# Kernel tuning notes

Hardware: AMD Instinct MI355X
Metric: run time of the kernel (lower is better)

## Reference

```python
import jax, jax.numpy as jnp
import numpy as np

NEG_SLOPE = 0.01  # torch F.leaky_relu default used in the DGL GAT-style layer


def grat_layer(h, src, dst, W, a, n_nodes):
    """One GRAT (GAT-style) layer.
    h: [N, d_in], src/dst: [E] int, W: [d_in, d_out], a: [2*d_out] (attn_fc weight
    on concat [z_src || z_dst]). Returns [N, d_out].
    """
    d_out = W.shape[1]
    z = h @ W                                   # [N, d_out]
    # attention logits per edge: a^T [z_src || z_dst]
    s_src = z @ a[:d_out]                       # [N]
    s_dst = z @ a[d_out:]                       # [N]
    e = jax.nn.leaky_relu(s_src[src] + s_dst[dst], NEG_SLOPE)  # [E]
    # numerically stable softmax over incoming edges of each dst node
    m = jax.ops.segment_max(e, dst, num_segments=n_nodes)      # [N]
    m = jnp.where(jnp.isfinite(m), m, 0.0)      # nodes with no in-edges
    w = jnp.exp(e - m[dst])                     # [E]
    denom = jax.ops.segment_sum(w, dst, num_segments=n_nodes)  # [N]
    alpha = w / jnp.maximum(denom, 1e-9)[dst]   # [E]
    # weighted scatter-aggregate of source features into dst
    out = jax.ops.segment_sum(alpha[:, None] * z[src], dst, num_segments=n_nodes)
    return out                                  # [N, d_out]


def setup_inputs() -> dict:
    key = jax.random.key(0)
    ks = jax.random.split(key, 10)
    N, E = 100000, 1600000
    IN, H1, H2, OUT = 128, 32, 32, 1
    feature = jax.random.normal(ks[0], (N, IN), dtype=jnp.float32)
    src = jax.random.randint(ks[1], (E,), 0, N, dtype=jnp.int32)
    dst = jax.random.randint(ks[2], (E,), 0, N, dtype=jnp.int32)
    s = 0.1
    W1 = jax.random.normal(ks[3], (IN, H1), dtype=jnp.float32) * s
    a1 = jax.random.normal(ks[4], (2 * H1,), dtype=jnp.float32) * s
    W2 = jax.random.normal(ks[5], (H1, H2), dtype=jnp.float32) * s
    a2 = jax.random.normal(ks[6], (2 * H2,), dtype=jnp.float32) * s
    W3 = jax.random.normal(ks[7], (H2, OUT), dtype=jnp.float32) * s
    a3 = jax.random.normal(ks[8], (2 * OUT,), dtype=jnp.float32) * s
    return {"feature": feature, "src": src, "dst": dst,
            "W1": W1, "a1": a1, "W2": W2, "a2": a2, "W3": W3, "a3": a3}


def reference(feature, src, dst, W1, a1, W2, a2, W3, a3):
    n = feature.shape[0]
    h = jax.nn.relu(grat_layer(feature, src, dst, W1, a1, n))
    h = jax.nn.relu(grat_layer(h, src, dst, W2, a2, n))
    h = grat_layer(h, src, dst, W3, a3, n)
    return jax.nn.sigmoid(h)                    # [N, 1]
```

## Files before the change

kernel.cpp:

```cpp
#include <hip/hip_runtime.h>
#include <hip/hip_bf16.h>
#include <cstdint>
#include <cstddef>

#define NEG_SLOPE 0.01f

static __device__ __forceinline__ unsigned short f2bf(float f) {
    __hip_bfloat16 b = __float2bfloat16(f);
    return *(unsigned short*)&b;
}


__global__ __launch_bounds__(128) void gemm1_kernel(
    const float* __restrict__ h, const float* __restrict__ W,
    const float* __restrict__ a, unsigned short* __restrict__ zb,
    float* __restrict__ s_src, float* __restrict__ s_dst, int N)
{
    __shared__ float Wl[128 * 32];
    int tid = threadIdx.x;
    int rowBase = blockIdx.x * 64;

    {
        const float4* W4 = (const float4*)W;
        float4* Wl4 = (float4*)Wl;
        for (int i = tid; i < 1024; i += 128) Wl4[i] = W4[i];
    }
    __syncthreads();

    int wv   = tid >> 6;
    int lane = tid & 63;
    int g    = lane >> 3;
    int l8   = lane & 7;
    int r0   = wv * 32 + g * 4;
    int col4 = l8 * 4;

    float acc[4][4];
#pragma unroll
    for (int i = 0; i < 4; i++)
#pragma unroll
        for (int c = 0; c < 4; c++) acc[i][c] = 0.f;

    const float4* h4  = (const float4*)h;
    const float4* Wl4 = (const float4*)Wl;

    size_t rowOff[4];
#pragma unroll
    for (int i = 0; i < 4; i++) {
        int r = rowBase + r0 + i;
        rowOff[i] = (size_t)((r < N) ? r : (N - 1)) * 32;
    }

#pragma unroll 2
    for (int kq = 0; kq < 32; kq++) {
        float4 w0 = Wl4[(kq * 4 + 0) * 8 + l8];
        float4 w1 = Wl4[(kq * 4 + 1) * 8 + l8];
        float4 w2 = Wl4[(kq * 4 + 2) * 8 + l8];
        float4 w3 = Wl4[(kq * 4 + 3) * 8 + l8];
#pragma unroll
        for (int i = 0; i < 4; i++) {
            float4 hv = h4[rowOff[i] + kq];
            acc[i][0] += hv.x * w0.x; acc[i][1] += hv.x * w0.y;
            acc[i][2] += hv.x * w0.z; acc[i][3] += hv.x * w0.w;
            acc[i][0] += hv.y * w1.x; acc[i][1] += hv.y * w1.y;
            acc[i][2] += hv.y * w1.z; acc[i][3] += hv.y * w1.w;
            acc[i][0] += hv.z * w2.x; acc[i][1] += hv.z * w2.y;
            acc[i][2] += hv.z * w2.z; acc[i][3] += hv.z * w2.w;
            acc[i][0] += hv.w * w3.x; acc[i][1] += hv.w * w3.y;
            acc[i][2] += hv.w * w3.z; acc[i][3] += hv.w * w3.w;
        }
    }

    float4 alo = ((const float4*)a)[l8];
    float4 ahi = ((const float4*)a)[8 + l8];
#pragma unroll
    for (int i = 0; i < 4; i++) {
        int row = rowBase + r0 + i;
        if (row < N) {
            ushort4 zv4 = make_ushort4(f2bf(acc[i][0]), f2bf(acc[i][1]),
                                       f2bf(acc[i][2]), f2bf(acc[i][3]));
            *(ushort4*)&zb[(size_t)row * 32 + col4] = zv4;
            float ps = acc[i][0] * alo.x + acc[i][1] * alo.y + acc[i][2] * alo.z + acc[i][3] * alo.w;
            float pd = acc[i][0] * ahi.x + acc[i][1] * ahi.y + acc[i][2] * ahi.z + acc[i][3] * ahi.w;
            ps += __shfl_xor(ps, 1, 64); ps += __shfl_xor(ps, 2, 64); ps += __shfl_xor(ps, 4, 64);
            pd += __shfl_xor(pd, 1, 64); pd += __shfl_xor(pd, 2, 64); pd += __shfl_xor(pd, 4, 64);
            if (l8 == 0) { s_src[row] = ps; s_dst[row] = pd; }
        }
    }
}


#define TILE_E 4096
#define NB_MAX 512

__global__ __launch_bounds__(256) void csr_hist_kernel(
    const int* __restrict__ dst, int* __restrict__ counts,
    int E, int TB, int NB)
{
    __shared__ int hist[NB_MAX];
    int tid = threadIdx.x;
    int t = blockIdx.x;
    for (int b = tid; b < NB; b += 256) hist[b] = 0;
    __syncthreads();
    int base = t * TILE_E;
    for (int i = tid; i < TILE_E; i += 256) {
        int k = base + i;
        if (k < E) atomicAdd(&hist[dst[k] >> 8], 1);
    }
    __syncthreads();
    for (int b = tid; b < NB; b += 256) counts[b * TB + t] = hist[b];
}

__global__ __launch_bounds__(256) void scan1_kernel(
    const int* __restrict__ vals, int* __restrict__ incl,
    int* __restrict__ blockSums, int M)
{
    __shared__ int tmp[256];
    int tid = threadIdx.x;
    int i = blockIdx.x * 256 + tid;
    int v = (i < M) ? vals[i] : 0;
    tmp[tid] = v;
    __syncthreads();
#pragma unroll
    for (int off = 1; off < 256; off <<= 1) {
        int t = (tid >= off) ? tmp[tid - off] : 0;
        __syncthreads();
        tmp[tid] += t;
        __syncthreads();
    }
    if (i < M) incl[i] = tmp[tid];
    if (tid == 255) blockSums[blockIdx.x] = tmp[255];
}

__global__ __launch_bounds__(256) void scan3_kernel(
    const int* __restrict__ vals, const int* __restrict__ blockSums,
    int* __restrict__ cscan, int M, int E)
{
    __shared__ int red[256];
    int tid = threadIdx.x;
    int bid = blockIdx.x;
    int partial = 0;
    for (int j = tid; j < bid; j += 256) partial += blockSums[j];
    red[tid] = partial;
    __syncthreads();
#pragma unroll
    for (int off = 128; off > 0; off >>= 1) {
        if (tid < off) red[tid] += red[tid + off];
        __syncthreads();
    }
    int prefix = red[0];
    int i = bid * 256 + tid;
    if (i < M) cscan[i] = cscan[i] - vals[i] + prefix;
    if (i == 0) cscan[M] = E;
}

__global__ __launch_bounds__(256) void csr_scatter_kernel(
    const int* __restrict__ src, const int* __restrict__ dst,
    const int* __restrict__ cscan, int* __restrict__ ebuf,
    int E, int TB, int NB)
{
    __shared__ int baseB[NB_MAX];
    __shared__ int cur[NB_MAX];
    int tid = threadIdx.x;
    int t = blockIdx.x;
    for (int b = tid; b < NB; b += 256) {
        baseB[b] = cscan[b * TB + t];
        cur[b] = 0;
    }
    __syncthreads();
    int base = t * TILE_E;
    for (int i = tid; i < TILE_E; i += 256) {
        int k = base + i;
        if (k < E) {
            int d = dst[k], s = src[k];
            int b = d >> 8;
            int r = atomicAdd(&cur[b], 1);
            ebuf[baseB[b] + r] = (s << 8) | (d & 255);
        }
    }
}

__global__ __launch_bounds__(256) void csr_bucket_kernel(
    const int* __restrict__ ebuf, const int* __restrict__ cscan,
    int* __restrict__ csr_src, int* __restrict__ offsets,
    int N, int E, int TB)
{
    __shared__ int eb[8192];
    __shared__ int hist[256];
    __shared__ int loff[256];
    __shared__ int tmp[256];
    int tid = threadIdx.x;
    int b = blockIdx.x;

    int beg = cscan[b * TB];
    int endv = cscan[(b + 1) * TB];
    int cnt = endv - beg;
    int first = b << 8;

    hist[tid] = 0;
    __syncthreads();

    bool inLds = (cnt <= 8192);
    for (int i = tid; i < cnt; i += 256) {
        int v = ebuf[beg + i];
        if (inLds) eb[i] = v;
        atomicAdd(&hist[v & 255], 1);
    }
    __syncthreads();

    int hv = hist[tid];
    tmp[tid] = hv;
    __syncthreads();
#pragma unroll
    for (int off = 1; off < 256; off <<= 1) {
        int t = (tid >= off) ? tmp[tid - off] : 0;
        __syncthreads();
        tmp[tid] += t;
        __syncthreads();
    }
    loff[tid] = tmp[tid] - hv;
    __syncthreads();

    if (first + tid < N) offsets[first + tid] = beg + loff[tid];
    if (b == 0 && tid == 0) offsets[N] = E;

    hist[tid] = 0;
    __syncthreads();

    for (int i = tid; i < cnt; i += 256) {
        int v = inLds ? eb[i] : ebuf[beg + i];
        int d8 = v & 255;
        int r = atomicAdd(&hist[d8], 1);
        csr_src[beg + loff[d8] + r] = v >> 8;
    }
}


#define AGG32_CORE(S_SRC, S_DST, ZB)                                          \
    int beg = offsets[node], end = offsets[node + 1];                         \
    int deg = end - beg;                                                      \
    float sd = (S_DST)[node];                                                 \
    int q  = lane >> 3;                                                       \
    int c4 = (lane & 7) * 4;                                                  \
    unsigned cb = (unsigned)(lane & 7) * 8u;                                  \
    const char* zbc = (const char*)(ZB);                                      \
    float4 o4 = make_float4(0.f, 0.f, 0.f, 0.f);                              \
    float rden;                                                               \
    if (deg <= 32) {                                                          \
        int p = beg + lane;                                                   \
        int vld = (p < end);                                                  \
        int s = vld ? csr_src[p] : 0;                                         \
        float sval = (S_SRC)[s];            \
        int soff = s << 6;                                                    \
        int e0 = __shfl(soff, q + 0,  32);                                    \
        int e1 = __shfl(soff, q + 4,  32);                                    \
        int e2 = __shfl(soff, q + 8,  32);                                    \
        int e3 = __shfl(soff, q + 12, 32);                                    \
        uint2 g0 = *(const uint2*)(zbc + (cb + (unsigned)e0));                \
        uint2 g1 = *(const uint2*)(zbc + (cb + (unsigned)e1));                \
        uint2 g2 = *(const uint2*)(zbc + (cb + (unsigned)e2));                \
        uint2 g3 = *(const uint2*)(zbc + (cb + (unsigned)e3));                \
        float e = -3.0e38f;                                                   \
        if (vld) {                                                            \
            e = sval + sd;                                                    \
            e = (e > 0.f) ? e : NEG_SLOPE * e;                                \
        }                                                                     \
        float m = e;                                                          \
        _Pragma("unroll")                                                     \
        for (int off = 16; off > 0; off >>= 1)                                \
            m = fmaxf(m, __shfl_xor(m, off, 32));                             \
        float w = vld ? __expf(e - m) : 0.f;                                  \
        float l = w;                                                          \
        _Pragma("unroll")                                                     \
        for (int off = 16; off > 0; off >>= 1) l += __shfl_xor(l, off, 32);   \
        rden = 1.f / fmaxf(l, 1e-9f);                                         \
        uint2 g4, g5, g6, g7;                                                 \
        if (deg > 16) {         \
            int e4 = __shfl(soff, q + 16, 32);                                \
            int e5 = __shfl(soff, q + 20, 32);                                \
            int e6 = __shfl(soff, q + 24, 32);                                \
            int e7 = __shfl(soff, q + 28, 32);                                \
            g4 = *(const uint2*)(zbc + (cb + (unsigned)e4));                  \
            g5 = *(const uint2*)(zbc + (cb + (unsigned)e5));                  \
            g6 = *(const uint2*)(zbc + (cb + (unsigned)e6));                  \
            g7 = *(const uint2*)(zbc + (cb + (unsigned)e7));                  \
        }                                                                     \
        float w0 = __shfl(w, q + 0,  32);                                     \
        float w1 = __shfl(w, q + 4,  32);                                     \
        float w2 = __shfl(w, q + 8,  32);                                     \
        float w3 = __shfl(w, q + 12, 32);                                     \
        o4.x += w0 * __uint_as_float(g0.x << 16);                             \
        o4.y += w0 * __uint_as_float(g0.x & 0xffff0000u);                     \
        o4.z += w0 * __uint_as_float(g0.y << 16);                             \
        o4.w += w0 * __uint_as_float(g0.y & 0xffff0000u);                     \
        o4.x += w1 * __uint_as_float(g1.x << 16);                             \
        o4.y += w1 * __uint_as_float(g1.x & 0xffff0000u);                     \
        o4.z += w1 * __uint_as_float(g1.y << 16);                             \
        o4.w += w1 * __uint_as_float(g1.y & 0xffff0000u);                     \
        o4.x += w2 * __uint_as_float(g2.x << 16);                             \
        o4.y += w2 * __uint_as_float(g2.x & 0xffff0000u);                     \
        o4.z += w2 * __uint_as_float(g2.y << 16);                             \
        o4.w += w2 * __uint_as_float(g2.y & 0xffff0000u);                     \
        o4.x += w3 * __uint_as_float(g3.x << 16);                             \
        o4.y += w3 * __uint_as_float(g3.x & 0xffff0000u);                     \
        o4.z += w3 * __uint_as_float(g3.y << 16);                             \
        o4.w += w3 * __uint_as_float(g3.y & 0xffff0000u);                     \
        if (deg > 16) {                                                       \
            float w4 = __shfl(w, q + 16, 32);                                 \
            float w5 = __shfl(w, q + 20, 32);                                 \
            float w6 = __shfl(w, q + 24, 32);                                 \
            float w7 = __shfl(w, q + 28, 32);                                 \
            o4.x += w4 * __uint_as_float(g4.x << 16);                         \
            o4.y += w4 * __uint_as_float(g4.x & 0xffff0000u);                 \
            o4.z += w4 * __uint_as_float(g4.y << 16);                         \
            o4.w += w4 * __uint_as_float(g4.y & 0xffff0000u);                 \
            o4.x += w5 * __uint_as_float(g5.x << 16);                         \
            o4.y += w5 * __uint_as_float(g5.x & 0xffff0000u);                 \
            o4.z += w5 * __uint_as_float(g5.y << 16);                         \
            o4.w += w5 * __uint_as_float(g5.y & 0xffff0000u);                 \
            o4.x += w6 * __uint_as_float(g6.x << 16);                         \
            o4.y += w6 * __uint_as_float(g6.x & 0xffff0000u);                 \
            o4.z += w6 * __uint_as_float(g6.y << 16);                         \
            o4.w += w6 * __uint_as_float(g6.y & 0xffff0000u);                 \
            o4.x += w7 * __uint_as_float(g7.x << 16);                         \
            o4.y += w7 * __uint_as_float(g7.x & 0xffff0000u);                 \
            o4.z += w7 * __uint_as_float(g7.y << 16);                         \
            o4.w += w7 * __uint_as_float(g7.y & 0xffff0000u);                 \
        }                                                                     \
    } else if (deg <= 128) {                                                  \
        int   sreg[4];                                                        \
        float ev[4];                                                          \
        int nIter = (deg + 31) >> 5;                                          \
        float m = -3.0e38f;                                                   \
        _Pragma("unroll 4")                                                   \
        for (int it = 0; it < nIter; ++it) {                                  \
            int p = beg + it * 32 + lane;                                     \
            float e = -3.0e38f;                                               \
            int s = 0;                                                        \
            if (p < end) {                                                    \
                s = csr_src[p];                                               \
                e = (S_SRC)[s] + sd;                                          \
                e = (e > 0.f) ? e : NEG_SLOPE * e;                            \
            }                                                                 \
            sreg[it] = s << 6;                                                \
            ev[it] = e;                                                       \
            m = fmaxf(m, e);                                                  \
        }                                                                     \
        _Pragma("unroll")                                                     \
        for (int off = 16; off > 0; off >>= 1)                                \
            m = fmaxf(m, __shfl_xor(m, off, 32));                             \
        float l = 0.f;                                                        \
        _Pragma("unroll 4")                                                   \
        for (int it = 0; it < nIter; ++it) {                                  \
            int p = beg + it * 32 + lane;                                     \
            float w = (p < end) ? __expf(ev[it] - m) : 0.f;                   \
            ws[it * 32 + lane] = make_float2(w, __int_as_float(sreg[it]));    \
            l += w;                                                           \
        }                                                                     \
        _Pragma("unroll")                                                     \
        for (int off = 16; off > 0; off >>= 1) l += __shfl_xor(l, off, 32);   \
        rden = 1.f / fmaxf(l, 1e-9f);                                         \
        int degP = (deg + 3) & ~3;                                            \
        int p = 0;                                                            \
        for (; p + 16 <= degP; p += 16) {                                     \
            float2 a0 = ws[p +      q], a1 = ws[p + 4  + q];                  \
            float2 a2 = ws[p + 8  + q], a3 = ws[p + 12 + q];                  \
            uint2 u0 = *(const uint2*)(zbc + (cb + (unsigned)__float_as_int(a0.y))); \
            uint2 u1 = *(const uint2*)(zbc + (cb + (unsigned)__float_as_int(a1.y))); \
            uint2 u2 = *(const uint2*)(zbc + (cb + (unsigned)__float_as_int(a2.y))); \
            uint2 u3 = *(const uint2*)(zbc + (cb + (unsigned)__float_as_int(a3.y))); \
            o4.x += a0.x * __uint_as_float(u0.x << 16);                       \
            o4.y += a0.x * __uint_as_float(u0.x & 0xffff0000u);               \
            o4.z += a0.x * __uint_as_float(u0.y << 16);                       \
            o4.w += a0.x * __uint_as_float(u0.y & 0xffff0000u);               \
            o4.x += a1.x * __uint_as_float(u1.x << 16);                       \
            o4.y += a1.x * __uint_as_float(u1.x & 0xffff0000u);               \
            o4.z += a1.x * __uint_as_float(u1.y << 16);                       \
            o4.w += a1.x * __uint_as_float(u1.y & 0xffff0000u);               \
            o4.x += a2.x * __uint_as_float(u2.x << 16);                       \
            o4.y += a2.x * __uint_as_float(u2.x & 0xffff0000u);               \
            o4.z += a2.x * __uint_as_float(u2.y << 16);                       \
            o4.w += a2.x * __uint_as_float(u2.y & 0xffff0000u);               \
            o4.x += a3.x * __uint_as_float(u3.x << 16);                       \
            o4.y += a3.x * __uint_as_float(u3.x & 0xffff0000u);               \
            o4.z += a3.x * __uint_as_float(u3.y << 16);                       \
            o4.w += a3.x * __uint_as_float(u3.y & 0xffff0000u);               \
        }                                                                     \
        for (; p < degP; p += 4) {                                            \
            float2 aa = ws[p + q];                                            \
            uint2 u = *(const uint2*)(zbc + (cb + (unsigned)__float_as_int(aa.y))); \
            o4.x += aa.x * __uint_as_float(u.x << 16);                        \
            o4.y += aa.x * __uint_as_float(u.x & 0xffff0000u);                \
            o4.z += aa.x * __uint_as_float(u.y << 16);                        \
            o4.w += aa.x * __uint_as_float(u.y & 0xffff0000u);                \
        }                                                                     \
    } else {                                                                  \
        float m = -3.0e38f;                                                   \
        for (int p = beg + lane; p < end; p += 32) {                          \
            float e = (S_SRC)[csr_src[p]] + sd;                               \
            e = (e > 0.f) ? e : NEG_SLOPE * e;                                \
            m = fmaxf(m, e);                                                  \
        }                                                                     \
        _Pragma("unroll")                                                     \
        for (int off = 16; off > 0; off >>= 1)                                \
            m = fmaxf(m, __shfl_xor(m, off, 32));                             \
        float l = 0.f;                                                        \
        for (int p = beg + lane; p < end; p += 32) {                          \
            float e = (S_SRC)[csr_src[p]] + sd;                               \
            e = (e > 0.f) ? e : NEG_SLOPE * e;                                \
            l += __expf(e - m);                                               \
        }                                                                     \
        _Pragma("unroll")                                                     \
        for (int off = 16; off > 0; off >>= 1) l += __shfl_xor(l, off, 32);   \
        rden = 1.f / fmaxf(l, 1e-9f);                                         \
        for (int p = 0; p < deg; p += 4) {                                    \
            int idx = p + q;                                                  \
            int valid = (idx < deg);                                          \
            int s = csr_src[beg + (valid ? idx : deg - 1)];                   \
            float e = (S_SRC)[s] + sd;                                        \
            e = (e > 0.f) ? e : NEG_SLOPE * e;                                \
            float w = valid ? __expf(e - m) : 0.f;                            \
            uint2 u = *(const uint2*)(zbc + (cb + ((unsigned)s << 6)));       \
            o4.x += w * __uint_as_float(u.x << 16);                           \
            o4.y += w * __uint_as_float(u.x & 0xffff0000u);                   \
            o4.z += w * __uint_as_float(u.y << 16);                           \
            o4.w += w * __uint_as_float(u.y & 0xffff0000u);                   \
        }                                                                     \
    }                                                                         \
    o4.x += __shfl_xor(o4.x, 8, 32);                                          \
    o4.y += __shfl_xor(o4.y, 8, 32);                                          \
    o4.z += __shfl_xor(o4.z, 8, 32);                                          \
    o4.w += __shfl_xor(o4.w, 8, 32);                                          \
    o4.x += __shfl_xor(o4.x, 16, 32);                                         \
    o4.y += __shfl_xor(o4.y, 16, 32);                                         \
    o4.z += __shfl_xor(o4.z, 16, 32);                                         \
    o4.w += __shfl_xor(o4.w, 16, 32);                                         \
    float4 vv4;                                                               \
    vv4.x = fmaxf(o4.x * rden, 0.f);                                          \
    vv4.y = fmaxf(o4.y * rden, 0.f);                                          \
    vv4.z = fmaxf(o4.z * rden, 0.f);                                          \
    vv4.w = fmaxf(o4.w * rden, 0.f);

__global__ __launch_bounds__(256) void agg32_l1_kernel(
    const int* __restrict__ offsets, const int* __restrict__ csr_src,
    const float* __restrict__ s_src1, const float* __restrict__ s_dst1,
    const unsigned short* __restrict__ zb1,
    const float* __restrict__ W2, const float* __restrict__ a2,
    unsigned short* __restrict__ zb2,
    float* __restrict__ s_src2, float* __restrict__ s_dst2, int N)
{
    __shared__ float W2l[32 * 32];
    __shared__ float2 wsbuf[8 * 128];
    __shared__ float hl[8 * 32];
    int tid = threadIdx.x;
    for (int i = tid; i < 1024; i += 256) W2l[i] = W2[i];
    __syncthreads();

    int g    = tid >> 5;
    int lane = tid & 31;
    int node = blockIdx.x * 8 + g;
    if (node >= N) return;
    float2* ws = &wsbuf[g * 128];

    AGG32_CORE(s_src1, s_dst1, zb1)

    if (q == 0) *(float4*)&hl[g * 32 + c4] = vv4;
    const float4* hb4 = (const float4*)&hl[g * 32];
    float acc2 = 0.f;
#pragma unroll
    for (int c = 0; c < 8; ++c) {
        float4 hv = hb4[c];
        acc2 += hv.x * W2l[(c * 4 + 0) * 32 + lane];
        acc2 += hv.y * W2l[(c * 4 + 1) * 32 + lane];
        acc2 += hv.z * W2l[(c * 4 + 2) * 32 + lane];
        acc2 += hv.w * W2l[(c * 4 + 3) * 32 + lane];
    }

    zb2[(size_t)node * 32 + lane] = f2bf(acc2);
    float ps = acc2 * a2[lane];
    float pd = acc2 * a2[32 + lane];
#pragma unroll
    for (int off = 16; off > 0; off >>= 1) {
        ps += __shfl_xor(ps, off, 32);
        pd += __shfl_xor(pd, off, 32);
    }
    if (lane == 0) { s_src2[node] = ps; s_dst2[node] = pd; }
}

__global__ __launch_bounds__(256) void agg32_l2_kernel(
    const int* __restrict__ offsets, const int* __restrict__ csr_src,
    const float* __restrict__ s_src2, const float* __restrict__ s_dst2,
    const unsigned short* __restrict__ zb2,
    const float* __restrict__ W3, const float* __restrict__ a3,
    float2* __restrict__ zs, float* __restrict__ s_dst3, int N)
{
    __shared__ float2 wsbuf[8 * 128];
    int tid  = threadIdx.x;
    int g    = tid >> 5;
    int lane = tid & 31;
    int node = blockIdx.x * 8 + g;
    if (node >= N) return;
    float2* ws = &wsbuf[g * 128];

    AGG32_CORE(s_src2, s_dst2, zb2)

    float4 w3q = ((const float4*)W3)[lane & 7];
    float t = vv4.x * w3q.x + vv4.y * w3q.y + vv4.z * w3q.z + vv4.w * w3q.w;
    t += __shfl_xor(t, 1, 32);
    t += __shfl_xor(t, 2, 32);
    t += __shfl_xor(t, 4, 32);
    if (lane == 0) {
        zs[node] = make_float2(t, t * a3[0]);
        s_dst3[node] = t * a3[1];
    }
}

__global__ __launch_bounds__(256) void agg1_fused_kernel(
    const int* __restrict__ offsets, const int* __restrict__ csr_src,
    const float2* __restrict__ zs, const float* __restrict__ s_dst,
    float* __restrict__ out, int N)
{
    int node = blockIdx.x * 8 + (threadIdx.x >> 5);
    int lane = threadIdx.x & 31;
    if (node >= N) return;

    int beg = offsets[node], end = offsets[node + 1];
    int deg = end - beg;
    float sd = s_dst[node];

    if (deg <= 128) {
        float ev[4], zv[4];
        int nIter = (deg + 31) >> 5;
        float m = -3.0e38f;
#pragma unroll 4
        for (int it = 0; it < nIter; ++it) {
            int p = beg + it * 32 + lane;
            float e = -3.0e38f, zz = 0.f;
            if (p < end) {
                float2 v2 = zs[csr_src[p]];
                zz = v2.x;
                e = v2.y + sd;
                e = (e > 0.f) ? e : NEG_SLOPE * e;
            }
            ev[it] = e; zv[it] = zz;
            m = fmaxf(m, e);
        }
#pragma unroll
        for (int off = 16; off > 0; off >>= 1) m = fmaxf(m, __shfl_xor(m, off, 32));
        float l = 0.f, o = 0.f;
#pragma unroll 4
        for (int it = 0; it < nIter; ++it) {
            int p = beg + it * 32 + lane;
            float w = (p < end) ? __expf(ev[it] - m) : 0.f;
            l += w;
            o += w * zv[it];
        }
#pragma unroll
        for (int off = 16; off > 0; off >>= 1) {
            l += __shfl_xor(l, off, 32);
            o += __shfl_xor(o, off, 32);
        }
        if (lane == 0) {
            float v = o / fmaxf(l, 1e-9f);
            out[node] = 1.f / (1.f + __expf(-v));
        }
    } else {
        float m = -3.0e38f;
        for (int p = beg + lane; p < end; p += 32) {
            float e = zs[csr_src[p]].y + sd;
            e = (e > 0.f) ? e : NEG_SLOPE * e;
            m = fmaxf(m, e);
        }
#pragma unroll
        for (int off = 16; off > 0; off >>= 1) m = fmaxf(m, __shfl_xor(m, off, 32));
        float l = 0.f, o = 0.f;
        for (int p = beg + lane; p < end; p += 32) {
            float2 v2 = zs[csr_src[p]];
            float e = v2.y + sd;
            e = (e > 0.f) ? e : NEG_SLOPE * e;
            float w = __expf(e - m);
            l += w; o += w * v2.x;
        }
#pragma unroll
        for (int off = 16; off > 0; off >>= 1) {
            l += __shfl_xor(l, off, 32);
            o += __shfl_xor(o, off, 32);
        }
        if (lane == 0) {
            float v = o / fmaxf(l, 1e-9f);
            out[node] = 1.f / (1.f + __expf(-v));
        }
    }
}


extern "C" void kernel_launch(void* const* d_in, const int* in_sizes, int n_in,
                              void* d_out, int out_size, void* d_ws, size_t ws_size,
                              hipStream_t stream)
{
    const float* feature = (const float*)d_in[0];
    const int*   src     = (const int*)d_in[1];
    const int*   dst     = (const int*)d_in[2];
    const float* W1      = (const float*)d_in[3];
    const float* a1      = (const float*)d_in[4];
    const float* W2      = (const float*)d_in[5];
    const float* a2      = (const float*)d_in[6];
    const float* W3      = (const float*)d_in[7];
    const float* a3      = (const float*)d_in[8];
    float* out = (float*)d_out;

    const int N = in_sizes[0] / 128;
    const int E = in_sizes[1];

    const int TB = (E + TILE_E - 1) / TILE_E;
    const int NB = (N + 255) >> 8;
    const int M  = NB * TB;

    char* p = (char*)d_ws;
    unsigned short* zb1 = (unsigned short*)p;  p += (size_t)N * 32 * sizeof(unsigned short);
    unsigned short* zb2 = (unsigned short*)p;  p += (size_t)N * 32 * sizeof(unsigned short);
    float* zs32    = (float*)p;  p += (size_t)N * 2 * sizeof(float);
    float* s_src1  = (float*)p;  p += (size_t)N * sizeof(float);
    float* s_dst1  = (float*)p;  p += (size_t)N * sizeof(float);
    float* s_src2  = (float*)p;  p += (size_t)N * sizeof(float);
    float* s_dst2  = (float*)p;  p += (size_t)N * sizeof(float);
    float* s_dst3  = (float*)p;  p += (size_t)N * sizeof(float);
    int*   offsets = (int*)p;    p += ((size_t)N + 1) * sizeof(int);
    int*   counts  = (int*)p;    p += ((size_t)M + 1) * sizeof(int);
    int*   cscan   = (int*)p;    p += ((size_t)M + 1) * sizeof(int);
    int*   blockSums = (int*)p;  p += 1024 * sizeof(int);
    int*   ebuf    = (int*)p;    p += (size_t)E * sizeof(int);
    int*   csr_src = (int*)p;    p += (size_t)E * sizeof(int);

    const int nodeBlocks8  = (N + 7) / 8;
    const int gemmBlocks64 = (N + 63) / 64;
    const int scanBlocksM  = (M + 255) / 256;

    hipLaunchKernelGGL(csr_hist_kernel, dim3(TB), dim3(256), 0, stream,
                       dst, counts, E, TB, NB);
    hipLaunchKernelGGL(scan1_kernel, dim3(scanBlocksM), dim3(256), 0, stream,
                       counts, cscan, blockSums, M);
    hipLaunchKernelGGL(scan3_kernel, dim3(scanBlocksM), dim3(256), 0, stream,
                       counts, blockSums, cscan, M, E);
    hipLaunchKernelGGL(csr_scatter_kernel, dim3(TB), dim3(256), 0, stream,
                       src, dst, cscan, ebuf, E, TB, NB);
    hipLaunchKernelGGL(csr_bucket_kernel, dim3(NB), dim3(256), 0, stream,
                       ebuf, cscan, csr_src, offsets, N, E, TB);

    hipLaunchKernelGGL(gemm1_kernel, dim3(gemmBlocks64), dim3(128), 0, stream,
                       feature, W1, a1, zb1, s_src1, s_dst1, N);
    hipLaunchKernelGGL(agg32_l1_kernel, dim3(nodeBlocks8), dim3(256), 0, stream,
                       offsets, csr_src, s_src1, s_dst1, zb1, W2, a2,
                       zb2, s_src2, s_dst2, N);

    float2* zs = (float2*)zs32;
    hipLaunchKernelGGL(agg32_l2_kernel, dim3(nodeBlocks8), dim3(256), 0, stream,
                       offsets, csr_src, s_src2, s_dst2, zb2, W3, a3,
                       zs, s_dst3, N);

    hipLaunchKernelGGL(agg1_fused_kernel, dim3(nodeBlocks8), dim3(256), 0, stream,
                       offsets, csr_src, zs, s_dst3, out, N);
}
```

Before: 244.5 us.

## Store node features in fp32 instead of bf16 and prefetch edge data early

Switches the intermediate z feature buffers from bf16 to fp32, so the gathers in the aggregation kernels read float4 rows and no longer unpack bf16. It also moves the CSR offset, source-index and attention-score loads ahead of the W2 shared-memory staging and barrier in the layer-1 kernel, so their latency overlaps that setup. The gathers for edges 16 to 31 are issued before the softmax sum reduction to hide more latency. Each gather now moves twice as many bytes, which raises memory and cache traffic in a kernel that is likely bandwidth-bound, in exchange for better accuracy and less ALU work.

```diff
diff --git a/kernel.cpp b/kernel.cpp
--- a/kernel.cpp
+++ b/kernel.cpp
@@ -5,15 +5,10 @@
 
 #define NEG_SLOPE 0.01f
 
-static __device__ __forceinline__ unsigned short f2bf(float f) {
-    __hip_bfloat16 b = __float2bfloat16(f);
-    return *(unsigned short*)&b;
-}
-
 
 __global__ __launch_bounds__(128) void gemm1_kernel(
     const float* __restrict__ h, const float* __restrict__ W,
-    const float* __restrict__ a, unsigned short* __restrict__ zb,
+    const float* __restrict__ a, float* __restrict__ zb,
     float* __restrict__ s_src, float* __restrict__ s_dst, int N)
 {
     __shared__ float Wl[128 * 32];
@@ -76,9 +71,8 @@
     for (int i = 0; i < 4; i++) {
         int row = rowBase + r0 + i;
         if (row < N) {
-            ushort4 zv4 = make_ushort4(f2bf(acc[i][0]), f2bf(acc[i][1]),
-                                       f2bf(acc[i][2]), f2bf(acc[i][3]));
-            *(ushort4*)&zb[(size_t)row * 32 + col4] = zv4;
+            *(float4*)&zb[(size_t)row * 32 + col4] =
+                make_float4(acc[i][0], acc[i][1], acc[i][2], acc[i][3]);
             float ps = acc[i][0] * alo.x + acc[i][1] * alo.y + acc[i][2] * alo.z + acc[i][3] * alo.w;
             float pd = acc[i][0] * ahi.x + acc[i][1] * ahi.y + acc[i][2] * ahi.z + acc[i][3] * ahi.w;
             ps += __shfl_xor(ps, 1, 64); ps += __shfl_xor(ps, 2, 64); ps += __shfl_xor(ps, 4, 64);
@@ -235,96 +229,76 @@
 }
 
 
+#define AGG32_PRELOAD(S_SRC, S_DST)                                           \
+    int nodeC = (node < N) ? node : (N - 1);                                  \
+    int beg = offsets[nodeC], end = offsets[nodeC + 1];                       \
+    int deg = end - beg;                                                      \
+    float sd = (S_DST)[nodeC];                                                \
+    int pfx = beg + lane;                                                     \
+    int s_pre = (deg <= 32 && pfx < end) ? csr_src[pfx] : 0;                  \
+    float sval_pre = (deg <= 32) ? (S_SRC)[s_pre] : 0.f;
+
 #define AGG32_CORE(S_SRC, S_DST, ZB)                                          \
-    int beg = offsets[node], end = offsets[node + 1];                         \
-    int deg = end - beg;                                                      \
-    float sd = (S_DST)[node];                                                 \
     int q  = lane >> 3;                                                       \
     int c4 = (lane & 7) * 4;                                                  \
-    unsigned cb = (unsigned)(lane & 7) * 8u;                                  \
+    unsigned cb = (unsigned)(lane & 7) * 16u;                                 \
     const char* zbc = (const char*)(ZB);                                      \
     float4 o4 = make_float4(0.f, 0.f, 0.f, 0.f);                              \
     float rden;                                                               \
     if (deg <= 32) {                                                          \
-        int p = beg + lane;                                                   \
-        int vld = (p < end);                                                  \
-        int s = vld ? csr_src[p] : 0;                                         \
-        float sval = (S_SRC)[s];            \
-        int soff = s << 6;                                                    \
+        int vld = (pfx < end);                                                \
+        int soff = s_pre << 7;                                                \
         int e0 = __shfl(soff, q + 0,  32);                                    \
         int e1 = __shfl(soff, q + 4,  32);                                    \
         int e2 = __shfl(soff, q + 8,  32);                                    \
         int e3 = __shfl(soff, q + 12, 32);                                    \
-        uint2 g0 = *(const uint2*)(zbc + (cb + (unsigned)e0));                \
-        uint2 g1 = *(const uint2*)(zbc + (cb + (unsigned)e1));                \
-        uint2 g2 = *(const uint2*)(zbc + (cb + (unsigned)e2));                \
-        uint2 g3 = *(const uint2*)(zbc + (cb + (unsigned)e3));                \
+        float4 g0 = *(const float4*)(zbc + (cb + (unsigned)e0));              \
+        float4 g1 = *(const float4*)(zbc + (cb + (unsigned)e1));              \
+        float4 g2 = *(const float4*)(zbc + (cb + (unsigned)e2));              \
+        float4 g3 = *(const float4*)(zbc + (cb + (unsigned)e3));              \
         float e = -3.0e38f;                                                   \
         if (vld) {                                                            \
-            e = sval + sd;                                                    \
+            e = sval_pre + sd;                                                \
             e = (e > 0.f) ? e : NEG_SLOPE * e;                                \
         }                                                                     \
         float m = e;                                                          \
         _Pragma("unroll")                                                     \
         for (int off = 16; off > 0; off >>= 1)                                \
             m = fmaxf(m, __shfl_xor(m, off, 32));                             \
+        int dgt = (deg > 16);                                                 \
+        float4 g4, g5, g6, g7;                                                \
+        if (dgt) {                \
+            int e4 = __shfl(soff, q + 16, 32);                                \
+            int e5 = __shfl(soff, q + 20, 32);                                \
+            int e6 = __shfl(soff, q + 24, 32);                                \
+            int e7 = __shfl(soff, q + 28, 32);                                \
+            g4 = *(const float4*)(zbc + (cb + (unsigned)e4));                 \
+            g5 = *(const float4*)(zbc + (cb + (unsigned)e5));                 \
+            g6 = *(const float4*)(zbc + (cb + (unsigned)e6));                 \
+            g7 = *(const float4*)(zbc + (cb + (unsigned)e7));                 \
+        }                                                                     \
         float w = vld ? __expf(e - m) : 0.f;                                  \
         float l = w;                                                          \
         _Pragma("unroll")                                                     \
         for (int off = 16; off > 0; off >>= 1) l += __shfl_xor(l, off, 32);   \
         rden = 1.f / fmaxf(l, 1e-9f);                                         \
-        uint2 g4, g5, g6, g7;                                                 \
-        if (deg > 16) {         \
-            int e4 = __shfl(soff, q + 16, 32);                                \
-            int e5 = __shfl(soff, q + 20, 32);                                \
-            int e6 = __shfl(soff, q + 24, 32);                                \
-            int e7 = __shfl(soff, q + 28, 32);                                \
-            g4 = *(const uint2*)(zbc + (cb + (unsigned)e4));                  \
-            g5 = *(const uint2*)(zbc + (cb + (unsigned)e5));                  \
-            g6 = *(const uint2*)(zbc + (cb + (unsigned)e6));                  \
-            g7 = *(const uint2*)(zbc + (cb + (unsigned)e7));                  \
-        }                                                                     \
         float w0 = __shfl(w, q + 0,  32);                                     \
         float w1 = __shfl(w, q + 4,  32);                                     \
         float w2 = __shfl(w, q + 8,  32);                                     \
         float w3 = __shfl(w, q + 12, 32);                                     \
-        o4.x += w0 * __uint_as_float(g0.x << 16);                             \
-        o4.y += w0 * __uint_as_float(g0.x & 0xffff0000u);                     \
-        o4.z += w0 * __uint_as_float(g0.y << 16);                             \
-        o4.w += w0 * __uint_as_float(g0.y & 0xffff0000u);                     \
-        o4.x += w1 * __uint_as_float(g1.x << 16);                             \
-        o4.y += w1 * __uint_as_float(g1.x & 0xffff0000u);                     \
-        o4.z += w1 * __uint_as_float(g1.y << 16);                             \
-        o4.w += w1 * __uint_as_float(g1.y & 0xffff0000u);                     \
-        o4.x += w2 * __uint_as_float(g2.x << 16);                             \
-        o4.y += w2 * __uint_as_float(g2.x & 0xffff0000u);                     \
-        o4.z += w2 * __uint_as_float(g2.y << 16);                             \
-        o4.w += w2 * __uint_as_float(g2.y & 0xffff0000u);                     \
-        o4.x += w3 * __uint_as_float(g3.x << 16);                             \
-        o4.y += w3 * __uint_as_float(g3.x & 0xffff0000u);                     \
-        o4.z += w3 * __uint_as_float(g3.y << 16);                             \
-        o4.w += w3 * __uint_as_float(g3.y & 0xffff0000u);                     \
-        if (deg > 16) {                                                       \
+        o4.x += w0 * g0.x; o4.y += w0 * g0.y; o4.z += w0 * g0.z; o4.w += w0 * g0.w; \
+        o4.x += w1 * g1.x; o4.y += w1 * g1.y; o4.z += w1 * g1.z; o4.w += w1 * g1.w; \
+        o4.x += w2 * g2.x; o4.y += w2 * g2.y; o4.z += w2 * g2.z; o4.w += w2 * g2.w; \
+        o4.x += w3 * g3.x; o4.y += w3 * g3.y; o4.z += w3 * g3.z; o4.w += w3 * g3.w; \
+        if (dgt) {                                                            \
             float w4 = __shfl(w, q + 16, 32);                                 \
             float w5 = __shfl(w, q + 20, 32);                                 \
             float w6 = __shfl(w, q + 24, 32);                                 \
             float w7 = __shfl(w, q + 28, 32);                                 \
-            o4.x += w4 * __uint_as_float(g4.x << 16);                         \
-            o4.y += w4 * __uint_as_float(g4.x & 0xffff0000u);                 \
-            o4.z += w4 * __uint_as_float(g4.y << 16);                         \
-            o4.w += w4 * __uint_as_float(g4.y & 0xffff0000u);                 \
-            o4.x += w5 * __uint_as_float(g5.x << 16);                         \
-            o4.y += w5 * __uint_as_float(g5.x & 0xffff0000u);                 \
-            o4.z += w5 * __uint_as_float(g5.y << 16);                         \
-            o4.w += w5 * __uint_as_float(g5.y & 0xffff0000u);                 \
-            o4.x += w6 * __uint_as_float(g6.x << 16);                         \
-            o4.y += w6 * __uint_as_float(g6.x & 0xffff0000u);                 \
-            o4.z += w6 * __uint_as_float(g6.y << 16);                         \
-            o4.w += w6 * __uint_as_float(g6.y & 0xffff0000u);                 \
-            o4.x += w7 * __uint_as_float(g7.x << 16);                         \
-            o4.y += w7 * __uint_as_float(g7.x & 0xffff0000u);                 \
-            o4.z += w7 * __uint_as_float(g7.y << 16);                         \
-            o4.w += w7 * __uint_as_float(g7.y & 0xffff0000u);                 \
+            o4.x += w4 * g4.x; o4.y += w4 * g4.y; o4.z += w4 * g4.z; o4.w += w4 * g4.w; \
+            o4.x += w5 * g5.x; o4.y += w5 * g5.y; o4.z += w5 * g5.z; o4.w += w5 * g5.w; \
+            o4.x += w6 * g6.x; o4.y += w6 * g6.y; o4.z += w6 * g6.z; o4.w += w6 * g6.w; \
+            o4.x += w7 * g7.x; o4.y += w7 * g7.y; o4.z += w7 * g7.z; o4.w += w7 * g7.w; \
         }                                                                     \
     } else if (deg <= 128) {                                                  \
         int   sreg[4];                                                        \
@@ -341,7 +315,7 @@
                 e = (S_SRC)[s] + sd;                                          \
                 e = (e > 0.f) ? e : NEG_SLOPE * e;                            \
             }                                                                 \
-            sreg[it] = s << 6;                                                \
+            sreg[it] = s << 7;                                                \
             ev[it] = e;                                                       \
             m = fmaxf(m, e);                                                  \
         }                                                                     \
@@ -364,34 +338,19 @@
         for (; p + 16 <= degP; p += 16) {                                     \
             float2 a0 = ws[p +      q], a1 = ws[p + 4  + q];                  \
             float2 a2 = ws[p + 8  + q], a3 = ws[p + 12 + q];                  \
-            uint2 u0 = *(const uint2*)(zbc + (cb + (unsigned)__float_as_int(a0.y))); \
-            uint2 u1 = *(const uint2*)(zbc + (cb + (unsigned)__float_as_int(a1.y))); \
-            uint2 u2 = *(const uint2*)(zbc + (cb + (unsigned)__float_as_int(a2.y))); \
-            uint2 u3 = *(const uint2*)(zbc + (cb + (unsigned)__float_as_int(a3.y))); \
-            o4.x += a0.x * __uint_as_float(u0.x << 16);                       \
-            o4.y += a0.x * __uint_as_float(u0.x & 0xffff0000u);               \
-            o4.z += a0.x * __uint_as_float(u0.y << 16);                       \
-            o4.w += a0.x * __uint_as_float(u0.y & 0xffff0000u);               \
-            o4.x += a1.x * __uint_as_float(u1.x << 16);                       \
-            o4.y += a1.x * __uint_as_float(u1.x & 0xffff0000u);               \
-            o4.z += a1.x * __uint_as_float(u1.y << 16);                       \
-            o4.w += a1.x * __uint_as_float(u1.y & 0xffff0000u);               \
-            o4.x += a2.x * __uint_as_float(u2.x << 16);                       \
-            o4.y += a2.x * __uint_as_float(u2.x & 0xffff0000u);               \
-            o4.z += a2.x * __uint_as_float(u2.y << 16);                       \
-            o4.w += a2.x * __uint_as_float(u2.y & 0xffff0000u);               \
-            o4.x += a3.x * __uint_as_float(u3.x << 16);                       \
-            o4.y += a3.x * __uint_as_float(u3.x & 0xffff0000u);               \
-            o4.z += a3.x * __uint_as_float(u3.y << 16);                       \
-            o4.w += a3.x * __uint_as_float(u3.y & 0xffff0000u);               \
+            float4 u0 = *(const float4*)(zbc + (cb + (unsigned)__float_as_int(a0.y))); \
+            float4 u1 = *(const float4*)(zbc + (cb + (unsigned)__float_as_int(a1.y))); \
+            float4 u2 = *(const float4*)(zbc + (cb + (unsigned)__float_as_int(a2.y))); \
+            float4 u3 = *(const float4*)(zbc + (cb + (unsigned)__float_as_int(a3.y))); \
+            o4.x += a0.x * u0.x; o4.y += a0.x * u0.y; o4.z += a0.x * u0.z; o4.w += a0.x * u0.w; \
+            o4.x += a1.x * u1.x; o4.y += a1.x * u1.y; o4.z += a1.x * u1.z; o4.w += a1.x * u1.w; \
+            o4.x += a2.x * u2.x; o4.y += a2.x * u2.y; o4.z += a2.x * u2.z; o4.w += a2.x * u2.w; \
+            o4.x += a3.x * u3.x; o4.y += a3.x * u3.y; o4.z += a3.x * u3.z; o4.w += a3.x * u3.w; \
         }                                                                     \
         for (; p < degP; p += 4) {                                            \
             float2 aa = ws[p + q];                                            \
-            uint2 u = *(const uint2*)(zbc + (cb + (unsigned)__float_as_int(aa.y))); \
-            o4.x += aa.x * __uint_as_float(u.x << 16);                        \
-            o4.y += aa.x * __uint_as_float(u.x & 0xffff0000u);                \
-            o4.z += aa.x * __uint_as_float(u.y << 16);                        \
-            o4.w += aa.x * __uint_as_float(u.y & 0xffff0000u);                \
+            float4 u = *(const float4*)(zbc + (cb + (unsigned)__float_as_int(aa.y))); \
+            o4.x += aa.x * u.x; o4.y += aa.x * u.y; o4.z += aa.x * u.z; o4.w += aa.x * u.w; \
         }                                                                     \
     } else {                                                                  \
         float m = -3.0e38f;                                                   \
@@ -419,11 +378,8 @@
             float e = (S_SRC)[s] + sd;                                        \
             e = (e > 0.f) ? e : NEG_SLOPE * e;                                \
             float w = valid ? __expf(e - m) : 0.f;                            \
-            uint2 u = *(const uint2*)(zbc + (cb + ((unsigned)s << 6)));       \
-            o4.x += w * __uint_as_float(u.x << 16);                           \
-            o4.y += w * __uint_as_float(u.x & 0xffff0000u);                   \
-            o4.z += w * __uint_as_float(u.y << 16);                           \
-            o4.w += w * __uint_as_float(u.y & 0xffff0000u);                   \
+            float4 u = *(const float4*)(zbc + (cb + ((unsigned)s << 7)));     \
+            o4.x += w * u.x; o4.y += w * u.y; o4.z += w * u.z; o4.w += w * u.w; \
         }                                                                     \
     }                                                                         \
     o4.x += __shfl_xor(o4.x, 8, 32);                                          \
@@ -443,21 +399,24 @@
 __global__ __launch_bounds__(256) void agg32_l1_kernel(
     const int* __restrict__ offsets, const int* __restrict__ csr_src,
     const float* __restrict__ s_src1, const float* __restrict__ s_dst1,
-    const unsigned short* __restrict__ zb1,
+    const float* __restrict__ zb1,
     const float* __restrict__ W2, const float* __restrict__ a2,
-    unsigned short* __restrict__ zb2,
+    float* __restrict__ zb2,
     float* __restrict__ s_src2, float* __restrict__ s_dst2, int N)
 {
     __shared__ float W2l[32 * 32];
     __shared__ float2 wsbuf[8 * 128];
     __shared__ float hl[8 * 32];
-    int tid = threadIdx.x;
-    for (int i = tid; i < 1024; i += 256) W2l[i] = W2[i];
-    __syncthreads();
-
+    int tid  = threadIdx.x;
     int g    = tid >> 5;
     int lane = tid & 31;
     int node = blockIdx.x * 8 + g;
+
+    AGG32_PRELOAD(s_src1, s_dst1)
+
+    for (int i = tid; i < 1024; i += 256) W2l[i] = W2[i];
+    __syncthreads();
+
     if (node >= N) return;
     float2* ws = &wsbuf[g * 128];
 
@@ -475,7 +434,7 @@
         acc2 += hv.w * W2l[(c * 4 + 3) * 32 + lane];
     }
 
-    zb2[(size_t)node * 32 + lane] = f2bf(acc2);
+    zb2[(size_t)node * 32 + lane] = acc2;
     float ps = acc2 * a2[lane];
     float pd = acc2 * a2[32 + lane];
 #pragma unroll
@@ -489,7 +448,7 @@
 __global__ __launch_bounds__(256) void agg32_l2_kernel(
     const int* __restrict__ offsets, const int* __restrict__ csr_src,
     const float* __restrict__ s_src2, const float* __restrict__ s_dst2,
-    const unsigned short* __restrict__ zb2,
+    const float* __restrict__ zb2,
     const float* __restrict__ W3, const float* __restrict__ a3,
     float2* __restrict__ zs, float* __restrict__ s_dst3, int N)
 {
@@ -501,6 +460,7 @@
     if (node >= N) return;
     float2* ws = &wsbuf[g * 128];
 
+    AGG32_PRELOAD(s_src2, s_dst2)
     AGG32_CORE(s_src2, s_dst2, zb2)
 
     float4 w3q = ((const float4*)W3)[lane & 7];
@@ -616,8 +576,8 @@
     const int M  = NB * TB;
 
     char* p = (char*)d_ws;
-    unsigned short* zb1 = (unsigned short*)p;  p += (size_t)N * 32 * sizeof(unsigned short);
-    unsigned short* zb2 = (unsigned short*)p;  p += (size_t)N * 32 * sizeof(unsigned short);
+    float* zb1     = (float*)p;  p += (size_t)N * 32 * sizeof(float);
+    float* zb2     = (float*)p;  p += (size_t)N * 32 * sizeof(float);
     float* zs32    = (float*)p;  p += (size_t)N * 2 * sizeof(float);
     float* s_src1  = (float*)p;  p += (size_t)N * sizeof(float);
     float* s_dst1  = (float*)p;  p += (size_t)N * sizeof(float);
```

Result: no change. 247.3 us (+1.1%).
